# Performance work log

Measured on AMD Instinct MI355X. Metric: run time of the kernel, lower is better.

Reference implementation:

```python
import jax, jax.numpy as jnp
import numpy as np

D_MODEL = 1024
H = 16
D_K = D_MODEL // H
WINDOW = 256
NEG = -1.0e9


def setup_inputs() -> dict:
    key = jax.random.key(0)
    ks = jax.random.split(key, 12)
    B, S = 1, 4096
    scale = 1.0 / np.sqrt(D_MODEL)
    inp = {
        'q': jax.random.normal(ks[0], (B, S, D_MODEL), dtype=jnp.float32),
        'k': jax.random.normal(ks[1], (B, S, D_MODEL), dtype=jnp.float32),
        'v': jax.random.normal(ks[2], (B, S, D_MODEL), dtype=jnp.float32),
        'w_q': jax.random.normal(ks[3], (D_MODEL, D_MODEL), dtype=jnp.float32) * scale,
        'b_q': jnp.zeros((D_MODEL,), dtype=jnp.float32),
        'w_k': jax.random.normal(ks[4], (D_MODEL, D_MODEL), dtype=jnp.float32) * scale,
        'b_k': jnp.zeros((D_MODEL,), dtype=jnp.float32),
        'w_v': jax.random.normal(ks[5], (D_MODEL, D_MODEL), dtype=jnp.float32) * scale,
        'b_v': jnp.zeros((D_MODEL,), dtype=jnp.float32),
        'w_o': jax.random.normal(ks[6], (D_MODEL, D_MODEL), dtype=jnp.float32) * scale,
        'b_o': jnp.zeros((D_MODEL,), dtype=jnp.float32),
    }
    return inp


def _local_mask(seq_len: int, window_size: int) -> jnp.ndarray:
    left = (window_size - 1) // 2
    right = window_size - 1 - left
    row = jnp.arange(seq_len)[:, None]
    col = jnp.arange(seq_len)[None, :]
    return (col >= row - left) & (col <= row + right)  # [S, S] bool


def reference(q, k, v, w_q, b_q, w_k, b_k, w_v, b_v, w_o, b_o):
    B, Sq, _ = q.shape
    Sk = k.shape[1]
    # projections (torch Linear: x @ W.T + b) -> [B, h, S, d_k]
    query = (q @ w_q.T + b_q).reshape(B, Sq, H, D_K).transpose(0, 2, 1, 3)
    key = (k @ w_k.T + b_k).reshape(B, Sk, H, D_K).transpose(0, 2, 1, 3)
    value = (v @ w_v.T + b_v).reshape(B, Sk, H, D_K).transpose(0, 2, 1, 3)

    scores = jnp.einsum('bhqd,bhkd->bhqk', query, key) / jnp.sqrt(
        jnp.asarray(D_K, dtype=query.dtype))
    if Sq == Sk:
        mask = _local_mask(Sq, WINDOW)  # [S, S]
        scores = jnp.where(mask[None, None], scores, jnp.asarray(NEG, scores.dtype))
    attn = jax.nn.softmax(scores, axis=-1)
    x = jnp.einsum('bhqk,bhkd->bhqd', attn, value)
    x = x.transpose(0, 2, 1, 3).reshape(B, Sq, D_MODEL)
    return x @ w_o.T + b_o
```

## Files before the change

### kernel.cpp

```cpp
#include <hip/hip_runtime.h>

#define SEQ 4096
#define DM 1024
#define NH 16
#define DK 64

typedef _Float16 half8 __attribute__((ext_vector_type(8)));
typedef _Float16 half4v __attribute__((ext_vector_type(4)));
typedef float f32x4 __attribute__((ext_vector_type(4)));

#define MFMA16(a, b, c) __builtin_amdgcn_mfma_f32_16x16x32_f16((a), (b), (c), 0, 0, 0)

__global__ void cvt_all(const float* __restrict__ q, const float* __restrict__ k,
                        const float* __restrict__ v, const float* __restrict__ wq,
                        const float* __restrict__ wk, const float* __restrict__ wv,
                        const float* __restrict__ wo, _Float16* __restrict__ qh,
                        _Float16* __restrict__ kh, _Float16* __restrict__ vh,
                        _Float16* __restrict__ wqh, _Float16* __restrict__ wkh,
                        _Float16* __restrict__ wvh, _Float16* __restrict__ woh) {
    int z = blockIdx.y;
    const float* src;
    _Float16* dst;
    int n;
    switch (z) {
    case 0: src = q;  dst = qh;  n = SEQ * DM; break;
    case 1: src = k;  dst = kh;  n = SEQ * DM; break;
    case 2: src = v;  dst = vh;  n = SEQ * DM; break;
    case 3: src = wq; dst = wqh; n = DM * DM;  break;
    case 4: src = wk; dst = wkh; n = DM * DM;  break;
    case 5: src = wv; dst = wvh; n = DM * DM;  break;
    default: src = wo; dst = woh; n = DM * DM; break;
    }
    int idx = (blockIdx.x * 256 + threadIdx.x) * 4;
    if (idx >= n) return;
    float4 f = *(const float4*)(src + idx);
    half4v h;
    h[0] = (_Float16)f.x; h[1] = (_Float16)f.y; h[2] = (_Float16)f.z; h[3] = (_Float16)f.w;
    *(half4v*)(dst + idx) = h;
}

__device__ __forceinline__ void gemm128_core(const _Float16* __restrict__ A,
                                             const _Float16* __restrict__ B,
                                             const float* __restrict__ bias,
                                             void* __restrict__ Cout, int mode, float scale) {
    const int K = DM;
    const int N = DM;
    __shared__ _Float16 As[128 * 32];
    __shared__ _Float16 Bs[128 * 32];
    int tid = threadIdx.x;
    int wave = tid >> 6, lane = tid & 63;
    int quad = lane >> 4, l16 = lane & 15;
    int m0 = blockIdx.x * 128;
    int n0 = blockIdx.y * 128;
    int wr = (wave >> 1) * 64;
    int wc = (wave & 1) * 64;
    f32x4 acc[4][4] = {};
    int c0 = wave * 64 + lane;

    for (int k0 = 0; k0 < K; k0 += 32) {
#pragma unroll
        for (int j = 0; j < 2; ++j) {
            int c = c0 + j * 256;
            int row = c >> 2, cc = c & 3;
            const _Float16* ga = A + (size_t)(m0 + row) * K + k0 + cc * 8;
            const _Float16* gb = B + (size_t)(n0 + row) * K + k0 + cc * 8;
            __builtin_amdgcn_global_load_lds(
                (const __attribute__((address_space(1))) void*)ga,
                (__attribute__((address_space(3))) void*)(As + j * 2048 + wave * 512), 16, 0, 0);
            __builtin_amdgcn_global_load_lds(
                (const __attribute__((address_space(1))) void*)gb,
                (__attribute__((address_space(3))) void*)(Bs + j * 2048 + wave * 512), 16, 0, 0);
        }
        __syncthreads();
        half8 af[4], bf[4];
#pragma unroll
        for (int mi = 0; mi < 4; ++mi)
            af[mi] = *(const half8*)&As[(wr + mi * 16 + l16) * 32 + quad * 8];
#pragma unroll
        for (int ni = 0; ni < 4; ++ni)
            bf[ni] = *(const half8*)&Bs[(wc + ni * 16 + l16) * 32 + quad * 8];
#pragma unroll
        for (int mi = 0; mi < 4; ++mi)
#pragma unroll
            for (int ni = 0; ni < 4; ++ni)
                acc[mi][ni] = MFMA16(af[mi], bf[ni], acc[mi][ni]);
        __syncthreads();
    }

    float bs[4];
#pragma unroll
    for (int ni = 0; ni < 4; ++ni) bs[ni] = bias[n0 + wc + ni * 16 + l16];

    if (mode == 0) {
        _Float16* C = (_Float16*)Cout;
#pragma unroll
        for (int mi = 0; mi < 4; ++mi)
#pragma unroll
            for (int ni = 0; ni < 4; ++ni) {
                int m = m0 + wr + mi * 16 + quad * 4;
                int n = n0 + wc + ni * 16 + l16;
#pragma unroll
                for (int r = 0; r < 4; ++r)
                    C[(size_t)(m + r) * N + n] = (_Float16)((acc[mi][ni][r] + bs[ni]) * scale);
            }
    } else if (mode == 1) {
        _Float16* C = (_Float16*)Cout;
#pragma unroll
        for (int mi = 0; mi < 4; ++mi)
#pragma unroll
            for (int ni = 0; ni < 4; ++ni) {
                int m = m0 + wr + mi * 16 + quad * 4;
                int n = n0 + wc + ni * 16 + l16;
                half4v p;
#pragma unroll
                for (int r = 0; r < 4; ++r) p[r] = (_Float16)(acc[mi][ni][r] + bs[ni]);
                *(half4v*)(C + (size_t)n * SEQ + m) = p;
            }
    } else {
        float* C = (float*)Cout;
#pragma unroll
        for (int mi = 0; mi < 4; ++mi)
#pragma unroll
            for (int ni = 0; ni < 4; ++ni) {
                int m = m0 + wr + mi * 16 + quad * 4;
                int n = n0 + wc + ni * 16 + l16;
#pragma unroll
                for (int r = 0; r < 4; ++r)
                    C[(size_t)(m + r) * N + n] = acc[mi][ni][r] + bs[ni];
            }
    }
}

__global__ void gemm_qkv(const _Float16* __restrict__ qh, const _Float16* __restrict__ kh,
                         const _Float16* __restrict__ vh, const _Float16* __restrict__ wqh,
                         const _Float16* __restrict__ wkh, const _Float16* __restrict__ wvh,
                         const float* __restrict__ bq, const float* __restrict__ bk,
                         const float* __restrict__ bv, _Float16* __restrict__ Qo,
                         _Float16* __restrict__ Ko, _Float16* __restrict__ Vt) {
    int z = blockIdx.z;
    const _Float16 *A, *B;
    const float* bias;
    void* C;
    int mode;
    float scale;
    if (z == 0) { A = qh; B = wqh; bias = bq; C = Qo; mode = 0; scale = 0.125f; }
    else if (z == 1) { A = kh; B = wkh; bias = bk; C = Ko; mode = 0; scale = 1.0f; }
    else { A = vh; B = wvh; bias = bv; C = Vt; mode = 1; scale = 1.0f; }
    gemm128_core(A, B, bias, C, mode, scale);
}

__global__ void gemm_out(const _Float16* __restrict__ Xh, const _Float16* __restrict__ woh,
                         const float* __restrict__ bo, float* __restrict__ out) {
    gemm128_core(Xh, woh, bo, out, 2, 1.0f);
}

__global__ void attn_kernel(const _Float16* __restrict__ Q, const _Float16* __restrict__ K,
                            const _Float16* __restrict__ Vt, _Float16* __restrict__ X) {
    __shared__ _Float16 Pl[4][16][32];
    int tid = threadIdx.x;
    int wave = tid >> 6, lane = tid & 63;
    int quad = lane >> 4, l16 = lane & 15;
    int h = blockIdx.y;
    int q0 = blockIdx.x * 64 + wave * 16;

    const _Float16* Qp = Q + (size_t)(q0 + l16) * DM + h * DK + quad * 8;
    half8 aq0 = *(const half8*)(Qp);
    half8 aq1 = *(const half8*)(Qp + 32);

    float rowM[4], rowL[4];
    f32x4 o[4] = {};
#pragma unroll
    for (int r = 0; r < 4; ++r) { rowM[r] = -__builtin_inff(); rowL[r] = 0.f; }

    int kstart = (q0 > 127) ? ((q0 - 127) & ~31) : 0;
    int kend = q0 + 143;
    if (kend > SEQ - 1) kend = SEQ - 1;

    for (int kt = kstart; kt <= kend; kt += 32) {
        f32x4 s[2];
#pragma unroll
        for (int cf = 0; cf < 2; ++cf) {
            int krow = kt + cf * 16 + l16;
            const _Float16* Kp = K + (size_t)krow * DM + h * DK + quad * 8;
            half8 b0 = *(const half8*)(Kp);
            half8 b1 = *(const half8*)(Kp + 32);
            f32x4 z = {};
            z = MFMA16(aq0, b0, z);
            z = MFMA16(aq1, b1, z);
            s[cf] = z;
        }
        float mnew[4], alpha[4];
#pragma unroll
        for (int r = 0; r < 4; ++r) {
            int row = q0 + quad * 4 + r;
#pragma unroll
            for (int cf = 0; cf < 2; ++cf) {
                int key = kt + cf * 16 + l16;
                bool valid = (key >= row - 127) && (key <= row + 128);
                if (!valid) s[cf][r] = -1e30f;
            }
            float t = fmaxf(s[0][r], s[1][r]);
#pragma unroll
            for (int off = 1; off < 16; off <<= 1) t = fmaxf(t, __shfl_xor(t, off));
            mnew[r] = fmaxf(rowM[r], t);
            alpha[r] = __expf(rowM[r] - mnew[r]);
            float p0 = __expf(s[0][r] - mnew[r]);
            float p1 = __expf(s[1][r] - mnew[r]);
            Pl[wave][quad * 4 + r][l16] = (_Float16)p0;
            Pl[wave][quad * 4 + r][l16 + 16] = (_Float16)p1;
            float rs = p0 + p1;
#pragma unroll
            for (int off = 1; off < 16; off <<= 1) rs += __shfl_xor(rs, off);
            rowL[r] = rowL[r] * alpha[r] + rs;
            rowM[r] = mnew[r];
        }
#pragma unroll
        for (int ni = 0; ni < 4; ++ni)
#pragma unroll
            for (int r = 0; r < 4; ++r) o[ni][r] *= alpha[r];
        half8 ap = *(const half8*)&Pl[wave][l16][quad * 8];
#pragma unroll
        for (int ni = 0; ni < 4; ++ni) {
            const _Float16* Vp = Vt + (size_t)(h * DK + ni * 16 + l16) * SEQ + kt + quad * 8;
            half8 bv = *(const half8*)(Vp);
            o[ni] = MFMA16(ap, bv, o[ni]);
        }
    }

    float rinv[4];
#pragma unroll
    for (int r = 0; r < 4; ++r) rinv[r] = 1.0f / rowL[r];
#pragma unroll
    for (int ni = 0; ni < 4; ++ni) {
        int n = h * DK + ni * 16 + l16;
#pragma unroll
        for (int r = 0; r < 4; ++r) {
            int m = q0 + quad * 4 + r;
            X[(size_t)m * DM + n] = (_Float16)(o[ni][r] * rinv[r]);
        }
    }
}

extern "C" void kernel_launch(void* const* d_in, const int* in_sizes, int n_in, void* d_out,
                              int out_size, void* d_ws, size_t ws_size, hipStream_t stream) {
    const float* q  = (const float*)d_in[0];
    const float* k  = (const float*)d_in[1];
    const float* v  = (const float*)d_in[2];
    const float* wq = (const float*)d_in[3];
    const float* bq = (const float*)d_in[4];
    const float* wk = (const float*)d_in[5];
    const float* bk = (const float*)d_in[6];
    const float* wv = (const float*)d_in[7];
    const float* bv = (const float*)d_in[8];
    const float* wo = (const float*)d_in[9];
    const float* bo = (const float*)d_in[10];

    const size_t SZ_T = (size_t)SEQ * DM * sizeof(_Float16);
    const size_t SZ_W = (size_t)DM * DM * sizeof(_Float16);
    char* p = (char*)d_ws;
    _Float16* qh  = (_Float16*)(p);
    _Float16* kh  = (_Float16*)(p + SZ_T);
    _Float16* vh  = (_Float16*)(p + 2 * SZ_T);
    _Float16* wqh = (_Float16*)(p + 3 * SZ_T);
    _Float16* wkh = (_Float16*)(p + 3 * SZ_T + SZ_W);
    _Float16* wvh = (_Float16*)(p + 3 * SZ_T + 2 * SZ_W);
    _Float16* woh = (_Float16*)(p + 3 * SZ_T + 3 * SZ_W);
    _Float16* Qo  = (_Float16*)(p + 3 * SZ_T + 4 * SZ_W);
    _Float16* Ko  = (_Float16*)(p + 4 * SZ_T + 4 * SZ_W);
    _Float16* Vt  = (_Float16*)(p + 5 * SZ_T + 4 * SZ_W);
    _Float16* Xh  = qh;

    cvt_all<<<dim3(4096, 7), 256, 0, stream>>>(q, k, v, wq, wk, wv, wo, qh, kh, vh, wqh, wkh,
                                               wvh, woh);
    gemm_qkv<<<dim3(32, 8, 3), 256, 0, stream>>>(qh, kh, vh, wqh, wkh, wvh, bq, bk, bv, Qo, Ko,
                                                 Vt);
    attn_kernel<<<dim3(SEQ / 64, NH), 256, 0, stream>>>(Qo, Ko, Vt, Xh);
    gemm_out<<<dim3(32, 8), 256, 0, stream>>>(Xh, woh, bo, (float*)d_out);
}
```

Baseline: 219.7 us.

## Use single-pass softmax over fixed key tiles in attention and shrink output GEMM tile

The attention kernel replaces the online-softmax loop with a fully unrolled pass. It computes all 10 key tiles of scores into registers, finds the row max once, writes the probabilities to per-tile LDS slots, and then does the PV MFMAs. This removes the per-tile rescaling, the repeated shuffle reductions and the loop-carried dependency, at the cost of more registers and LDS. Separately, the GEMM core is templated on M tile size, and the output projection uses 64-row tiles, doubling its grid to 512 blocks to better fill the CUs.

After: 218.2 us. No clear change (-0.7%).

```diff
diff --git a/kernel.cpp b/kernel.cpp
--- a/kernel.cpp
+++ b/kernel.cpp
@@ -4,6 +4,7 @@
 #define DM 1024
 #define NH 16
 #define DK 64
+#define NT 10
 
 typedef _Float16 half8 __attribute__((ext_vector_type(8)));
 typedef _Float16 half4v __attribute__((ext_vector_type(4)));
@@ -39,48 +40,55 @@
     *(half4v*)(dst + idx) = h;
 }
 
-__device__ __forceinline__ void gemm128_core(const _Float16* __restrict__ A,
-                                             const _Float16* __restrict__ B,
-                                             const float* __restrict__ bias,
-                                             void* __restrict__ Cout, int mode, float scale) {
+template <int MT>
+__device__ __forceinline__ void gemm_core(const _Float16* __restrict__ A,
+                                          const _Float16* __restrict__ B,
+                                          const float* __restrict__ bias,
+                                          void* __restrict__ Cout, int mode, float scale) {
     const int K = DM;
     const int N = DM;
-    __shared__ _Float16 As[128 * 32];
+    constexpr int MI = MT / 32;
+    constexpr int ACH = MT / 64;
+    __shared__ _Float16 As[MT * 32];
     __shared__ _Float16 Bs[128 * 32];
     int tid = threadIdx.x;
     int wave = tid >> 6, lane = tid & 63;
     int quad = lane >> 4, l16 = lane & 15;
-    int m0 = blockIdx.x * 128;
+    int m0 = blockIdx.x * MT;
     int n0 = blockIdx.y * 128;
-    int wr = (wave >> 1) * 64;
+    int wr = (wave >> 1) * (MT / 2);
     int wc = (wave & 1) * 64;
-    f32x4 acc[4][4] = {};
-    int c0 = wave * 64 + lane;
+    f32x4 acc[MI][4] = {};
 
     for (int k0 = 0; k0 < K; k0 += 32) {
 #pragma unroll
-        for (int j = 0; j < 2; ++j) {
-            int c = c0 + j * 256;
+        for (int j = 0; j < ACH; ++j) {
+            int c = j * 256 + tid;
             int row = c >> 2, cc = c & 3;
             const _Float16* ga = A + (size_t)(m0 + row) * K + k0 + cc * 8;
-            const _Float16* gb = B + (size_t)(n0 + row) * K + k0 + cc * 8;
             __builtin_amdgcn_global_load_lds(
                 (const __attribute__((address_space(1))) void*)ga,
                 (__attribute__((address_space(3))) void*)(As + j * 2048 + wave * 512), 16, 0, 0);
+        }
+#pragma unroll
+        for (int j = 0; j < 2; ++j) {
+            int c = j * 256 + tid;
+            int row = c >> 2, cc = c & 3;
+            const _Float16* gb = B + (size_t)(n0 + row) * K + k0 + cc * 8;
             __builtin_amdgcn_global_load_lds(
                 (const __attribute__((address_space(1))) void*)gb,
                 (__attribute__((address_space(3))) void*)(Bs + j * 2048 + wave * 512), 16, 0, 0);
         }
         __syncthreads();
-        half8 af[4], bf[4];
-#pragma unroll
-        for (int mi = 0; mi < 4; ++mi)
+        half8 af[MI], bf[4];
+#pragma unroll
+        for (int mi = 0; mi < MI; ++mi)
             af[mi] = *(const half8*)&As[(wr + mi * 16 + l16) * 32 + quad * 8];
 #pragma unroll
         for (int ni = 0; ni < 4; ++ni)
             bf[ni] = *(const half8*)&Bs[(wc + ni * 16 + l16) * 32 + quad * 8];
 #pragma unroll
-        for (int mi = 0; mi < 4; ++mi)
+        for (int mi = 0; mi < MI; ++mi)
 #pragma unroll
             for (int ni = 0; ni < 4; ++ni)
                 acc[mi][ni] = MFMA16(af[mi], bf[ni], acc[mi][ni]);
@@ -94,7 +102,7 @@
     if (mode == 0) {
         _Float16* C = (_Float16*)Cout;
 #pragma unroll
-        for (int mi = 0; mi < 4; ++mi)
+        for (int mi = 0; mi < MI; ++mi)
 #pragma unroll
             for (int ni = 0; ni < 4; ++ni) {
                 int m = m0 + wr + mi * 16 + quad * 4;
@@ -106,7 +114,7 @@
     } else if (mode == 1) {
         _Float16* C = (_Float16*)Cout;
 #pragma unroll
-        for (int mi = 0; mi < 4; ++mi)
+        for (int mi = 0; mi < MI; ++mi)
 #pragma unroll
             for (int ni = 0; ni < 4; ++ni) {
                 int m = m0 + wr + mi * 16 + quad * 4;
@@ -119,7 +127,7 @@
     } else {
         float* C = (float*)Cout;
 #pragma unroll
-        for (int mi = 0; mi < 4; ++mi)
+        for (int mi = 0; mi < MI; ++mi)
 #pragma unroll
             for (int ni = 0; ni < 4; ++ni) {
                 int m = m0 + wr + mi * 16 + quad * 4;
@@ -146,17 +154,19 @@
     if (z == 0) { A = qh; B = wqh; bias = bq; C = Qo; mode = 0; scale = 0.125f; }
     else if (z == 1) { A = kh; B = wkh; bias = bk; C = Ko; mode = 0; scale = 1.0f; }
     else { A = vh; B = wvh; bias = bv; C = Vt; mode = 1; scale = 1.0f; }
-    gemm128_core(A, B, bias, C, mode, scale);
+    gemm_core<128>(A, B, bias, C, mode, scale);
 }
 
 __global__ void gemm_out(const _Float16* __restrict__ Xh, const _Float16* __restrict__ woh,
                          const float* __restrict__ bo, float* __restrict__ out) {
-    gemm128_core(Xh, woh, bo, out, 2, 1.0f);
-}
-
-__global__ void attn_kernel(const _Float16* __restrict__ Q, const _Float16* __restrict__ K,
-                            const _Float16* __restrict__ Vt, _Float16* __restrict__ X) {
-    __shared__ _Float16 Pl[4][16][32];
+    gemm_core<64>(Xh, woh, bo, out, 2, 1.0f);
+}
+
+__global__ void __launch_bounds__(256) attn_kernel(const _Float16* __restrict__ Q,
+                                                   const _Float16* __restrict__ K,
+                                                   const _Float16* __restrict__ Vt,
+                                                   _Float16* __restrict__ X) {
+    __shared__ _Float16 Pl[4][NT][16][40];
     int tid = threadIdx.x;
     int wave = tid >> 6, lane = tid & 63;
     int quad = lane >> 4, l16 = lane & 15;
@@ -167,69 +177,75 @@
     half8 aq0 = *(const half8*)(Qp);
     half8 aq1 = *(const half8*)(Qp + 32);
 
-    float rowM[4], rowL[4];
-    f32x4 o[4] = {};
-#pragma unroll
-    for (int r = 0; r < 4; ++r) { rowM[r] = -__builtin_inff(); rowL[r] = 0.f; }
-
     int kstart = (q0 > 127) ? ((q0 - 127) & ~31) : 0;
-    int kend = q0 + 143;
-    if (kend > SEQ - 1) kend = SEQ - 1;
-
-    for (int kt = kstart; kt <= kend; kt += 32) {
-        f32x4 s[2];
+
+    f32x4 s[NT][2];
+#pragma unroll
+    for (int t = 0; t < NT; ++t) {
+        int kt = kstart + t * 32;
 #pragma unroll
         for (int cf = 0; cf < 2; ++cf) {
             int krow = kt + cf * 16 + l16;
-            const _Float16* Kp = K + (size_t)krow * DM + h * DK + quad * 8;
+            int kc = krow < SEQ ? krow : SEQ - 1;
+            const _Float16* Kp = K + (size_t)kc * DM + h * DK + quad * 8;
             half8 b0 = *(const half8*)(Kp);
             half8 b1 = *(const half8*)(Kp + 32);
             f32x4 z = {};
             z = MFMA16(aq0, b0, z);
             z = MFMA16(aq1, b1, z);
-            s[cf] = z;
-        }
-        float mnew[4], alpha[4];
-#pragma unroll
-        for (int r = 0; r < 4; ++r) {
-            int row = q0 + quad * 4 + r;
-#pragma unroll
-            for (int cf = 0; cf < 2; ++cf) {
-                int key = kt + cf * 16 + l16;
-                bool valid = (key >= row - 127) && (key <= row + 128);
-                if (!valid) s[cf][r] = -1e30f;
-            }
-            float t = fmaxf(s[0][r], s[1][r]);
-#pragma unroll
-            for (int off = 1; off < 16; off <<= 1) t = fmaxf(t, __shfl_xor(t, off));
-            mnew[r] = fmaxf(rowM[r], t);
-            alpha[r] = __expf(rowM[r] - mnew[r]);
-            float p0 = __expf(s[0][r] - mnew[r]);
-            float p1 = __expf(s[1][r] - mnew[r]);
-            Pl[wave][quad * 4 + r][l16] = (_Float16)p0;
-            Pl[wave][quad * 4 + r][l16 + 16] = (_Float16)p1;
-            float rs = p0 + p1;
-#pragma unroll
-            for (int off = 1; off < 16; off <<= 1) rs += __shfl_xor(rs, off);
-            rowL[r] = rowL[r] * alpha[r] + rs;
-            rowM[r] = mnew[r];
-        }
-#pragma unroll
-        for (int ni = 0; ni < 4; ++ni)
-#pragma unroll
-            for (int r = 0; r < 4; ++r) o[ni][r] *= alpha[r];
-        half8 ap = *(const half8*)&Pl[wave][l16][quad * 8];
+            s[t][cf] = z;
+        }
+    }
+
+#pragma unroll
+    for (int t = 0; t < NT; ++t)
+#pragma unroll
+        for (int cf = 0; cf < 2; ++cf) {
+            int key = kstart + t * 32 + cf * 16 + l16;
+#pragma unroll
+            for (int r = 0; r < 4; ++r) {
+                int row = q0 + quad * 4 + r;
+                bool valid = (key >= row - 127) && (key <= row + 128) && (key < SEQ);
+                if (!valid) s[t][cf][r] = -1e30f;
+            }
+        }
+
+    float rinv[4];
+#pragma unroll
+    for (int r = 0; r < 4; ++r) {
+        float m = -1e30f;
+#pragma unroll
+        for (int t = 0; t < NT; ++t) m = fmaxf(m, fmaxf(s[t][0][r], s[t][1][r]));
+#pragma unroll
+        for (int off = 1; off < 16; off <<= 1) m = fmaxf(m, __shfl_xor(m, off));
+        float sum = 0.f;
+#pragma unroll
+        for (int t = 0; t < NT; ++t) {
+            float p0 = __expf(s[t][0][r] - m);
+            float p1 = __expf(s[t][1][r] - m);
+            Pl[wave][t][quad * 4 + r][l16] = (_Float16)p0;
+            Pl[wave][t][quad * 4 + r][l16 + 16] = (_Float16)p1;
+            sum += p0 + p1;
+        }
+#pragma unroll
+        for (int off = 1; off < 16; off <<= 1) sum += __shfl_xor(sum, off);
+        rinv[r] = 1.0f / sum;
+    }
+
+    f32x4 o[4] = {};
+#pragma unroll
+    for (int t = 0; t < NT; ++t) {
+        half8 ap = *(const half8*)&Pl[wave][t][l16][quad * 8];
+        int vcol = kstart + t * 32 + quad * 8;
+        int vc = vcol < SEQ ? vcol : 0;
 #pragma unroll
         for (int ni = 0; ni < 4; ++ni) {
-            const _Float16* Vp = Vt + (size_t)(h * DK + ni * 16 + l16) * SEQ + kt + quad * 8;
+            const _Float16* Vp = Vt + (size_t)(h * DK + ni * 16 + l16) * SEQ + vc;
             half8 bv = *(const half8*)(Vp);
             o[ni] = MFMA16(ap, bv, o[ni]);
         }
     }
 
-    float rinv[4];
-#pragma unroll
-    for (int r = 0; r < 4; ++r) rinv[r] = 1.0f / rowL[r];
 #pragma unroll
     for (int ni = 0; ni < 4; ++ni) {
         int n = h * DK + ni * 16 + l16;
@@ -275,5 +291,5 @@
     gemm_qkv<<<dim3(32, 8, 3), 256, 0, stream>>>(qh, kh, vh, wqh, wkh, wvh, bq, bk, bv, Qo, Ko,
                                                  Vt);
     attn_kernel<<<dim3(SEQ / 64, NH), 256, 0, stream>>>(Qo, Ko, Vt, Xh);
-    gemm_out<<<dim3(32, 8), 256, 0, stream>>>(Xh, woh, bo, (float*)d_out);
-}
+    gemm_out<<<dim3(64, 8), 256, 0, stream>>>(Xh, woh, bo, (float*)d_out);
+}
```

## Deepen GEMM K-step to 64, shrink output GEMM tile, swizzle attention blocks

Applied to the files above, without the earlier changes.

Each GEMM loop iteration now loads a K-depth of 64 (two 32-wide slabs) per barrier pair, halving the number of syncthreads per tile. The output projection uses 64x128 tiles, giving twice as many workgroups for the 256-CU device. Launch bounds of 3 waves per SIMD are added, and attention workgroups are remapped with a block swizzle to change which query tiles run together. The cost is more LDS per block and possible register pressure from the launch bounds.

New measurement: 213.6 us. -2.8%, faster.

```diff
diff --git a/kernel.cpp b/kernel.cpp
--- a/kernel.cpp
+++ b/kernel.cpp
@@ -10,6 +10,9 @@
 typedef float f32x4 __attribute__((ext_vector_type(4)));
 
 #define MFMA16(a, b, c) __builtin_amdgcn_mfma_f32_16x16x32_f16((a), (b), (c), 0, 0, 0)
+#define GLOAD_LDS(g, l)                                                                  \
+    __builtin_amdgcn_global_load_lds((const __attribute__((address_space(1))) void*)(g), \
+                                     (__attribute__((address_space(3))) void*)(l), 16, 0, 0)
 
 __global__ void cvt_all(const float* __restrict__ q, const float* __restrict__ k,
                         const float* __restrict__ v, const float* __restrict__ wq,
@@ -39,60 +42,84 @@
     *(half4v*)(dst + idx) = h;
 }
 
-__device__ __forceinline__ void gemm128_core(const _Float16* __restrict__ A,
-                                             const _Float16* __restrict__ B,
-                                             const float* __restrict__ bias,
-                                             void* __restrict__ Cout, int mode, float scale) {
-    const int K = DM;
-    const int N = DM;
-    __shared__ _Float16 As[128 * 32];
-    __shared__ _Float16 Bs[128 * 32];
-    int tid = threadIdx.x;
-    int wave = tid >> 6, lane = tid & 63;
-    int quad = lane >> 4, l16 = lane & 15;
+template <int MT>
+__device__ __forceinline__ void gemm_bk64(const _Float16* __restrict__ A,
+                                          const _Float16* __restrict__ B, int m0, int n0,
+                                          _Float16* As, _Float16* Bs, f32x4 (*acc)[4]) {
+    constexpr int MI = MT / 32;
+    constexpr int ACH = MT / 64;
+    const int tid = threadIdx.x;
+    const int wave = tid >> 6, lane = tid & 63;
+    const int quad = lane >> 4, l16 = lane & 15;
+    const int wr = (wave >> 1) * (MT / 2);
+    const int wc = (wave & 1) * 64;
+    const int srow = tid >> 2, scol = (tid & 3) * 8;
+
+    for (int k0 = 0; k0 < DM; k0 += 64) {
+#pragma unroll
+        for (int p = 0; p < 2; ++p) {
+            int kc = k0 + p * 32 + scol;
+#pragma unroll
+            for (int j = 0; j < ACH; ++j)
+                GLOAD_LDS(A + (size_t)(m0 + j * 64 + srow) * DM + kc,
+                          As + p * (MT * 32) + j * 2048 + tid * 8);
+#pragma unroll
+            for (int j = 0; j < 2; ++j)
+                GLOAD_LDS(B + (size_t)(n0 + j * 64 + srow) * DM + kc,
+                          Bs + p * 4096 + j * 2048 + tid * 8);
+        }
+        __syncthreads();
+#pragma unroll
+        for (int p = 0; p < 2; ++p) {
+            half8 af[MI], bf[4];
+#pragma unroll
+            for (int mi = 0; mi < MI; ++mi)
+                af[mi] = *(const half8*)&As[p * (MT * 32) + (wr + mi * 16 + l16) * 32 + quad * 8];
+#pragma unroll
+            for (int ni = 0; ni < 4; ++ni)
+                bf[ni] = *(const half8*)&Bs[p * 4096 + (wc + ni * 16 + l16) * 32 + quad * 8];
+#pragma unroll
+            for (int mi = 0; mi < MI; ++mi)
+#pragma unroll
+                for (int ni = 0; ni < 4; ++ni)
+                    acc[mi][ni] = MFMA16(af[mi], bf[ni], acc[mi][ni]);
+        }
+        __syncthreads();
+    }
+}
+
+__global__ void __launch_bounds__(256, 3) gemm_qkv(
+    const _Float16* __restrict__ qh, const _Float16* __restrict__ kh,
+    const _Float16* __restrict__ vh, const _Float16* __restrict__ wqh,
+    const _Float16* __restrict__ wkh, const _Float16* __restrict__ wvh,
+    const float* __restrict__ bq, const float* __restrict__ bk, const float* __restrict__ bv,
+    _Float16* __restrict__ Qo, _Float16* __restrict__ Ko, _Float16* __restrict__ Vt) {
+    __shared__ _Float16 As[2 * 128 * 32];
+    __shared__ _Float16 Bs[2 * 128 * 32];
+    int z = blockIdx.z;
+    const _Float16 *A, *B;
+    const float* bias;
+    float scale;
+    if (z == 0) { A = qh; B = wqh; bias = bq; scale = 0.125f; }
+    else if (z == 1) { A = kh; B = wkh; bias = bk; scale = 1.0f; }
+    else { A = vh; B = wvh; bias = bv; scale = 1.0f; }
+
     int m0 = blockIdx.x * 128;
     int n0 = blockIdx.y * 128;
-    int wr = (wave >> 1) * 64;
-    int wc = (wave & 1) * 64;
     f32x4 acc[4][4] = {};
-    int c0 = wave * 64 + lane;
-
-    for (int k0 = 0; k0 < K; k0 += 32) {
-#pragma unroll
-        for (int j = 0; j < 2; ++j) {
-            int c = c0 + j * 256;
-            int row = c >> 2, cc = c & 3;
-            const _Float16* ga = A + (size_t)(m0 + row) * K + k0 + cc * 8;
-            const _Float16* gb = B + (size_t)(n0 + row) * K + k0 + cc * 8;
-            __builtin_amdgcn_global_load_lds(
-                (const __attribute__((address_space(1))) void*)ga,
-                (__attribute__((address_space(3))) void*)(As + j * 2048 + wave * 512), 16, 0, 0);
-            __builtin_amdgcn_global_load_lds(
-                (const __attribute__((address_space(1))) void*)gb,
-                (__attribute__((address_space(3))) void*)(Bs + j * 2048 + wave * 512), 16, 0, 0);
-        }
-        __syncthreads();
-        half8 af[4], bf[4];
-#pragma unroll
-        for (int mi = 0; mi < 4; ++mi)
-            af[mi] = *(const half8*)&As[(wr + mi * 16 + l16) * 32 + quad * 8];
-#pragma unroll
-        for (int ni = 0; ni < 4; ++ni)
-            bf[ni] = *(const half8*)&Bs[(wc + ni * 16 + l16) * 32 + quad * 8];
-#pragma unroll
-        for (int mi = 0; mi < 4; ++mi)
-#pragma unroll
-            for (int ni = 0; ni < 4; ++ni)
-                acc[mi][ni] = MFMA16(af[mi], bf[ni], acc[mi][ni]);
-        __syncthreads();
-    }
-
+    gemm_bk64<128>(A, B, m0, n0, As, Bs, acc);
+
+    const int tid = threadIdx.x;
+    const int wave = tid >> 6, lane = tid & 63;
+    const int quad = lane >> 4, l16 = lane & 15;
+    const int wr = (wave >> 1) * 64;
+    const int wc = (wave & 1) * 64;
     float bs[4];
 #pragma unroll
     for (int ni = 0; ni < 4; ++ni) bs[ni] = bias[n0 + wc + ni * 16 + l16];
 
-    if (mode == 0) {
-        _Float16* C = (_Float16*)Cout;
+    if (z < 2) {
+        _Float16* C = (z == 0) ? Qo : Ko;
 #pragma unroll
         for (int mi = 0; mi < 4; ++mi)
 #pragma unroll
@@ -101,10 +128,9 @@
                 int n = n0 + wc + ni * 16 + l16;
 #pragma unroll
                 for (int r = 0; r < 4; ++r)
-                    C[(size_t)(m + r) * N + n] = (_Float16)((acc[mi][ni][r] + bs[ni]) * scale);
+                    C[(size_t)(m + r) * DM + n] = (_Float16)((acc[mi][ni][r] + bs[ni]) * scale);
             }
-    } else if (mode == 1) {
-        _Float16* C = (_Float16*)Cout;
+    } else {
 #pragma unroll
         for (int mi = 0; mi < 4; ++mi)
 #pragma unroll
@@ -114,44 +140,37 @@
                 half4v p;
 #pragma unroll
                 for (int r = 0; r < 4; ++r) p[r] = (_Float16)(acc[mi][ni][r] + bs[ni]);
-                *(half4v*)(C + (size_t)n * SEQ + m) = p;
+                *(half4v*)(Vt + (size_t)n * SEQ + m) = p;
             }
-    } else {
-        float* C = (float*)Cout;
-#pragma unroll
-        for (int mi = 0; mi < 4; ++mi)
-#pragma unroll
-            for (int ni = 0; ni < 4; ++ni) {
-                int m = m0 + wr + mi * 16 + quad * 4;
-                int n = n0 + wc + ni * 16 + l16;
-#pragma unroll
-                for (int r = 0; r < 4; ++r)
-                    C[(size_t)(m + r) * N + n] = acc[mi][ni][r] + bs[ni];
-            }
-    }
-}
-
-__global__ void gemm_qkv(const _Float16* __restrict__ qh, const _Float16* __restrict__ kh,
-                         const _Float16* __restrict__ vh, const _Float16* __restrict__ wqh,
-                         const _Float16* __restrict__ wkh, const _Float16* __restrict__ wvh,
-                         const float* __restrict__ bq, const float* __restrict__ bk,
-                         const float* __restrict__ bv, _Float16* __restrict__ Qo,
-                         _Float16* __restrict__ Ko, _Float16* __restrict__ Vt) {
-    int z = blockIdx.z;
-    const _Float16 *A, *B;
-    const float* bias;
-    void* C;
-    int mode;
-    float scale;
-    if (z == 0) { A = qh; B = wqh; bias = bq; C = Qo; mode = 0; scale = 0.125f; }
-    else if (z == 1) { A = kh; B = wkh; bias = bk; C = Ko; mode = 0; scale = 1.0f; }
-    else { A = vh; B = wvh; bias = bv; C = Vt; mode = 1; scale = 1.0f; }
-    gemm128_core(A, B, bias, C, mode, scale);
-}
-
-__global__ void gemm_out(const _Float16* __restrict__ Xh, const _Float16* __restrict__ woh,
-                         const float* __restrict__ bo, float* __restrict__ out) {
-    gemm128_core(Xh, woh, bo, out, 2, 1.0f);
+    }
+}
+
+__global__ void __launch_bounds__(256, 3) gemm_out(const _Float16* __restrict__ Xh,
+                                                   const _Float16* __restrict__ woh,
+                                                   const float* __restrict__ bo,
+                                                   float* __restrict__ out) {
+    __shared__ _Float16 As[2 * 64 * 32];
+    __shared__ _Float16 Bs[2 * 128 * 32];
+    int m0 = blockIdx.x * 64;
+    int n0 = blockIdx.y * 128;
+    f32x4 acc[2][4] = {};
+    gemm_bk64<64>(Xh, woh, m0, n0, As, Bs, acc);
+
+    const int tid = threadIdx.x;
+    const int wave = tid >> 6, lane = tid & 63;
+    const int quad = lane >> 4, l16 = lane & 15;
+    const int wr = (wave >> 1) * 32;
+    const int wc = (wave & 1) * 64;
+#pragma unroll
+    for (int mi = 0; mi < 2; ++mi)
+#pragma unroll
+        for (int ni = 0; ni < 4; ++ni) {
+            int m = m0 + wr + mi * 16 + quad * 4;
+            int n = n0 + wc + ni * 16 + l16;
+            float b = bo[n];
+#pragma unroll
+            for (int r = 0; r < 4; ++r) out[(size_t)(m + r) * DM + n] = acc[mi][ni][r] + b;
+        }
 }
 
 __global__ void attn_kernel(const _Float16* __restrict__ Q, const _Float16* __restrict__ K,
@@ -161,7 +180,8 @@
     int wave = tid >> 6, lane = tid & 63;
     int quad = lane >> 4, l16 = lane & 15;
     int h = blockIdx.y;
-    int q0 = blockIdx.x * 64 + wave * 16;
+    int bx = ((blockIdx.x & 7) << 3) + (blockIdx.x >> 3);
+    int q0 = bx * 64 + wave * 16;
 
     const _Float16* Qp = Q + (size_t)(q0 + l16) * DM + h * DK + quad * 8;
     half8 aq0 = *(const half8*)(Qp);
@@ -275,5 +295,5 @@
     gemm_qkv<<<dim3(32, 8, 3), 256, 0, stream>>>(qh, kh, vh, wqh, wkh, wvh, bq, bk, bv, Qo, Ko,
                                                  Vt);
     attn_kernel<<<dim3(SEQ / 64, NH), 256, 0, stream>>>(Qo, Ko, Vt, Xh);
-    gemm_out<<<dim3(32, 8), 256, 0, stream>>>(Xh, woh, bo, (float*)d_out);
-}
+    gemm_out<<<dim3(64, 8), 256, 0, stream>>>(Xh, woh, bo, (float*)d_out);
+}
```
